# Kernel tuning notes

Hardware: AMD Instinct MI355X
Metric: run time of the kernel (lower is better)

Reference implementation:

```python
import jax, jax.numpy as jnp
import numpy as np

NUM_CLASSES = 80
ANCHORS = np.array([[10,13],[16,30],[33,23],[30,61],[62,45],[59,119],[116,90],[156,198],[373,326]], np.float32)
MASK = [[0,1,2],[3,4,5],[6,7,8]]
STRIDES = [8, 16, 32]
MAX_OUT = 100      # max_output_size_per_class == max_total_size
IOU_THR = 0.45
SCORE_THR = 0.25
NMS_TOPK = 128     # per-class candidate pre-selection for greedy NMS (>= MAX_OUT)


def setup_inputs() -> dict:
    key = jax.random.key(0)
    k1, k2, k3 = jax.random.split(key, 3)
    B = 16
    C = 3 * (NUM_CLASSES + 5)  # 255
    return {
        'p3': jax.random.normal(k1, (B, 80, 80, C), jnp.float32),
        'p4': jax.random.normal(k2, (B, 40, 40, C), jnp.float32),
        'p5': jax.random.normal(k3, (B, 20, 20, C), jnp.float32),
    }


def _decode(logits, anchors, stride):
    # logits: [B,H,W,3*(nc+5)] -> boxes [B,H*W*3,4] (x1y1x2y2), obj [B,M], cls [B,M,nc]
    B, H, W, _ = logits.shape
    A = anchors.shape[0]
    x = logits.reshape(B, H, W, A, NUM_CLASSES + 5)
    xy = jax.nn.sigmoid(x[..., :2])
    wh_logit = x[..., 2:4]
    obj = jax.nn.sigmoid(x[..., 4])
    cls = jax.nn.sigmoid(x[..., 5:])
    gx, gy = jnp.meshgrid(jnp.arange(W, dtype=x.dtype), jnp.arange(H, dtype=x.dtype))
    grid = jnp.stack([gx, gy], axis=-1)[:, :, None, :]  # [H,W,1,2]
    ctr = (xy + grid) * stride
    wh = jnp.exp(wh_logit) * anchors  # [B,H,W,A,2]
    box = jnp.concatenate([ctr - wh / 2.0, ctr + wh / 2.0], axis=-1)
    return box.reshape(B, -1, 4), obj.reshape(B, -1), cls.reshape(B, -1, NUM_CLASSES)


def _pairwise_iou(b):
    # b: [K,4] x1y1x2y2 -> [K,K]
    area = (b[:, 2] - b[:, 0]) * (b[:, 3] - b[:, 1])
    lt = jnp.maximum(b[:, None, :2], b[None, :, :2])
    rb = jnp.minimum(b[:, None, 2:], b[None, :, 2:])
    wh = jnp.clip(rb - lt, 0.0)
    inter = wh[..., 0] * wh[..., 1]
    return inter / (area[:, None] + area[None, :] - inter + 1e-9)


def _nms_single(boxes, scores):
    # boxes [N,4], scores [N] for one (image, class): greedy NMS on top-K candidates
    s = jnp.where(scores > SCORE_THR, scores, -1.0)
    top_s, idx = jax.lax.top_k(s, NMS_TOPK)   # sorted descending
    b = boxes[idx]                            # [K,4]
    iou = _pairwise_iou(b)                    # [K,K]
    rng = jnp.arange(NMS_TOPK)

    def body(keep, i):
        active = keep[i] & (top_s[i] > 0.0)
        sup = active & (iou[i] > IOU_THR) & (rng > i)
        return keep & ~sup, None

    keep, _ = jax.lax.scan(body, jnp.ones(NMS_TOPK, bool), rng)
    valid = keep & (top_s > 0.0)
    ss = jnp.where(valid, top_s, -1.0)
    sel_s, sel_i = jax.lax.top_k(ss, MAX_OUT)
    return b[sel_i], sel_s                    # [M,4], [M]


def _per_image(boxes, scores_cn):
    # boxes [N,4] shared across classes (q=1), scores_cn [C,N]
    cb, cs = jax.vmap(_nms_single, in_axes=(None, 0))(boxes, scores_cn)  # [C,M,4],[C,M]
    C = cs.shape[0]
    cls_id = jnp.broadcast_to(jnp.arange(C, dtype=boxes.dtype)[:, None], cs.shape)
    fs, fi = jax.lax.top_k(cs.reshape(-1), MAX_OUT)
    fb = cb.reshape(-1, 4)[fi]
    fc = cls_id.reshape(-1)[fi]
    valid = fs > 0.0
    n_valid = jnp.sum(valid).astype(jnp.int32)
    return (jnp.where(valid[:, None], fb, 0.0),
            jnp.where(valid, fs, 0.0),
            jnp.where(valid, fc, 0.0),
            n_valid)


def _forward(p3, p4, p5):
    boxes, objs, clss = [], [], []
    for logits, m, stride in zip((p3, p4, p5), MASK, STRIDES):
        b, o, c = _decode(logits, jnp.asarray(ANCHORS[m]), float(stride))
        boxes.append(b); objs.append(o); clss.append(c)
    boxes = jnp.concatenate(boxes, axis=1)   # [B,N,4]
    obj = jnp.concatenate(objs, axis=1)      # [B,N]
    cls = jnp.concatenate(clss, axis=1)      # [B,N,C]
    scores = obj[..., None] * cls            # [B,N,C]
    return jax.vmap(_per_image)(boxes, scores.transpose(0, 2, 1))


def reference(p3, p4, p5):
    # returns (boxes [B,100,4], scores [B,100], classes [B,100], valid [B])
    return _forward(p3, p4, p5)
```

## Files before the change

### kernel.cpp

```cpp
#include <hip/hip_runtime.h>
#include <stdint.h>

#define NUM_CLASSES 80
#define N_ANCH 25200
#define B_IMG 16
#define NMS_TOPK_ 128
#define MAX_OUT_ 100
#define SCORE_THR_ 0.25f
#define IOU_THR_ 0.45f
#define NBINS 2048
#define CAP 2048
#define CAPB 1024
#define CAPC 256
#define U16_THR 0x3E80u

__constant__ float c_anch[9][2] = {
    {10.f, 13.f}, {16.f, 30.f}, {33.f, 23.f},
    {30.f, 61.f}, {62.f, 45.f}, {59.f, 119.f},
    {116.f, 90.f}, {156.f, 198.f}, {373.f, 326.f}};

__device__ __forceinline__ float sigmoidf_(float x) {
    return 1.0f / (1.0f + expf(-x));
}

__device__ __forceinline__ unsigned int score_bin(unsigned int bits) {
    unsigned int bin = (bits - 0x3E800000u) >> 13;
    if (bin >= NBINS) bin = NBINS - 1;
    return bin;
}


__global__ void __launch_bounds__(256) decode_scores_u16_kernel(
    const float* __restrict__ p3, const float* __restrict__ p4,
    const float* __restrict__ p5, float* __restrict__ boxes,
    unsigned short* __restrict__ score_u) {
    int blk = blockIdx.x;
    int b = blk / 405;
    int tile = blk - b * 405;
    const float* p; int W, lvl, il0, base, ta;
    if (tile < 300)      { p = p3; W = 80; lvl = 0; ta = 64; il0 = tile * 64;         base = 0;     }
    else if (tile < 375) { p = p4; W = 40; lvl = 1; ta = 64; il0 = (tile - 300) * 64; base = 19200; }
    else                 { p = p5; W = 20; lvl = 2; ta = 40; il0 = (tile - 375) * 40; base = 24000; }
    float stride = (float)(8 << lvl);

    __shared__ float4 raw4[64 * 85 / 4];
    __shared__ float obj_sh[64];
    float* raw = (float*)raw4;
    int tid = threadIdx.x;

    const float4* src4 = (const float4*)(p + (size_t)b * ((size_t)W * W * 255) +
                                         (size_t)il0 * 85);
    int n4 = ta * 85 / 4;
    for (int k = tid; k < n4; k += 256) raw4[k] = src4[k];
    __syncthreads();

    if (tid < ta) {
        int il = il0 + tid;
        int y = il / (W * 3);
        int t = il - y * (W * 3);
        int x = t / 3;
        int a = t - x * 3;
        const float* q = &raw[tid * 85];
        float cx = (sigmoidf_(q[0]) + (float)x) * stride;
        float cy = (sigmoidf_(q[1]) + (float)y) * stride;
        float bw = expf(q[2]) * c_anch[lvl * 3 + a][0];
        float bh = expf(q[3]) * c_anch[lvl * 3 + a][1];
        int gi = base + il;
        float* bo = boxes + ((size_t)b * N_ANCH + gi) * 4;
        bo[0] = cx - bw * 0.5f; bo[1] = cy - bh * 0.5f;
        bo[2] = cx + bw * 0.5f; bo[3] = cy + bh * 0.5f;
        obj_sh[tid] = sigmoidf_(q[4]);
    }
    __syncthreads();

    int gi0 = base + il0;
    int gpc = ta >> 3;
    int ng = NUM_CLASSES * gpc;
    for (int o = tid; o < ng; o += 256) {
        int c, g;
        if (gpc == 8) { c = o >> 3; g = o & 7; }
        else          { c = o / 5;  g = o - c * 5; }
        int j = g * 8;
        unsigned int w[4];
#pragma unroll
        for (int k = 0; k < 4; ++k) {
            float s0 = obj_sh[j + 2 * k]     * sigmoidf_(raw[(j + 2 * k) * 85 + 5 + c]);
            float s1 = obj_sh[j + 2 * k + 1] * sigmoidf_(raw[(j + 2 * k + 1) * 85 + 5 + c]);
            w[k] = (__float_as_uint(s0) >> 16) | (__float_as_uint(s1) & 0xFFFF0000u);
        }
        uint4 v = {w[0], w[1], w[2], w[3]};
        *(uint4*)(score_u + ((size_t)(b * NUM_CLASSES + c)) * N_ANCH + gi0 + j) = v;
    }
}

__global__ void __launch_bounds__(256) select_topk_u16_kernel(
    const unsigned short* __restrict__ score_u,
    const float* __restrict__ p3, const float* __restrict__ p4,
    const float* __restrict__ p5,
    unsigned long long* __restrict__ topsel) {
    int bc = blockIdx.x;
    int b = bc / NUM_CLASSES;
    int c = bc - b * NUM_CLASSES;
    int tid = threadIdx.x;
    const uint4* sc = (const uint4*)(score_u + (size_t)bc * N_ANCH);

    __shared__ unsigned int hist[256];
    __shared__ unsigned long long sel[CAPB];
    __shared__ unsigned int s_cnt;
    __shared__ int s_cut;

    hist[tid] = 0u;
    if (tid == 0) s_cnt = 0u;
    __syncthreads();

    for (int i = tid; i < N_ANCH / 8; i += 256) {
        uint4 v = sc[i];
        unsigned int ww[4] = {v.x, v.y, v.z, v.w};
#pragma unroll
        for (int k = 0; k < 8; ++k) {
            unsigned int h = (ww[k >> 1] >> ((k & 1) * 16)) & 0xFFFFu;
            if (h >= U16_THR) {
                unsigned int bin = h - U16_THR;
                if (bin > 255u) bin = 255u;
                atomicAdd(&hist[bin], 1u);
            }
        }
    }
    __syncthreads();

    if (tid == 0) {
        unsigned int tot = 0; int cut = 0;
        for (int t = 255; t >= 0; --t) {
            tot += hist[t];
            if (tot >= NMS_TOPK_) { cut = t; break; }
        }
        s_cut = cut;
    }
    __syncthreads();
    unsigned int cutoff = (unsigned int)s_cut;

    for (int i = tid; i < N_ANCH / 8; i += 256) {
        uint4 v = sc[i];
        unsigned int ww[4] = {v.x, v.y, v.z, v.w};
#pragma unroll
        for (int k = 0; k < 8; ++k) {
            unsigned int h = (ww[k >> 1] >> ((k & 1) * 16)) & 0xFFFFu;
            if (h >= U16_THR) {
                unsigned int bin = h - U16_THR;
                if (bin > 255u) bin = 255u;
                if (bin >= cutoff) {
                    unsigned int pos = atomicAdd(&s_cnt, 1u);
                    if (pos < CAPB) sel[pos] = (unsigned long long)(i * 8 + k);
                }
            }
        }
    }
    __syncthreads();

    unsigned int M = s_cnt;
    if (M > CAPB) M = CAPB;

    for (unsigned int t = tid; t < M; t += 256) {
        unsigned int idx = (unsigned int)sel[t];
        const float* q;
        if (idx < 19200u)      q = p3 + (size_t)b * 1632000 + (size_t)idx * 85;
        else if (idx < 24000u) q = p4 + (size_t)b * 408000 + (size_t)(idx - 19200u) * 85;
        else                   q = p5 + (size_t)b * 102000 + (size_t)(idx - 24000u) * 85;
        float s = sigmoidf_(q[4]) * sigmoidf_(q[5 + c]);
        sel[t] = (s > SCORE_THR_)
                     ? (((unsigned long long)__float_as_uint(s) << 32) |
                        (unsigned long long)(~idx))
                     : 0ull;
    }
    __syncthreads();

    unsigned int P2 = 1;
    while (P2 < M) P2 <<= 1;
    if (P2 < 2) P2 = 2;
    for (unsigned int k = M + tid; k < P2; k += 256) sel[k] = 0ull;
    __syncthreads();

    for (unsigned int k = 2; k <= P2; k <<= 1) {
        for (unsigned int j = k >> 1; j > 0; j >>= 1) {
            for (unsigned int t = tid; t < (int)P2; t += 256) {
                unsigned int ixj = (unsigned int)t ^ j;
                if (ixj > (unsigned int)t) {
                    unsigned long long a0 = sel[t], b0 = sel[ixj];
                    bool desc = (((unsigned int)t & k) == 0);
                    if (desc ? (a0 < b0) : (a0 > b0)) { sel[t] = b0; sel[ixj] = a0; }
                }
            }
            __syncthreads();
        }
    }

    unsigned long long* dst = topsel + (size_t)bc * NMS_TOPK_;
    if (tid < NMS_TOPK_) dst[tid] = ((unsigned int)tid < M) ? sel[tid] : 0ull;
}

__global__ void __launch_bounds__(64) nms_kernel(
    const unsigned long long* __restrict__ topsel,
    const float* __restrict__ boxes,
    float* __restrict__ cls_score, float* __restrict__ cls_box) {
    int bc = blockIdx.x;
    int b = bc / NUM_CLASSES;
    unsigned int lane = threadIdx.x;

    __shared__ float bx[NMS_TOPK_][8];

    const unsigned long long* src = topsel + (size_t)bc * NMS_TOPK_;
    unsigned long long e0 = src[lane];
    unsigned long long e1 = src[64 + lane];

    bool k0 = (e0 != 0ull);
    bool k1 = (e1 != 0ull);

    float x00 = 0, y00 = 0, x01 = 0, y01 = 0, a0 = 0, sv0 = 0;
    float x10 = 0, y10 = 0, x11 = 0, y11 = 0, a1 = 0, sv1 = 0;
    if (k0) {
        unsigned int idx = ~((unsigned int)(e0 & 0xFFFFFFFFull));
        float4 bp = *(const float4*)(boxes + ((size_t)b * N_ANCH + idx) * 4);
        x00 = bp.x; y00 = bp.y; x01 = bp.z; y01 = bp.w;
        sv0 = __uint_as_float((unsigned int)(e0 >> 32));
        a0 = (x01 - x00) * (y01 - y00);
    }
    if (k1) {
        unsigned int idx = ~((unsigned int)(e1 & 0xFFFFFFFFull));
        float4 bp = *(const float4*)(boxes + ((size_t)b * N_ANCH + idx) * 4);
        x10 = bp.x; y10 = bp.y; x11 = bp.z; y11 = bp.w;
        sv1 = __uint_as_float((unsigned int)(e1 >> 32));
        a1 = (x11 - x10) * (y11 - y10);
    }
    {
        float4 v0 = {x00, y00, x01, y01};
        float4 v1 = {x10, y10, x11, y11};
        *(float4*)&bx[lane][0] = v0;
        *(float4*)&bx[64 + lane][0] = v1;
    }
    __syncthreads();

    unsigned long long km0 = __ballot(k0);
    unsigned long long km1 = __ballot(k1);
    for (unsigned int i = 0; i < NMS_TOPK_; ++i) {
        bool ki = ((((i < 64) ? km0 : km1) >> (i & 63)) & 1ull) != 0ull;
        if (ki) {
            float4 rb = *(const float4*)&bx[i][0];
            float ra = (rb.z - rb.x) * (rb.w - rb.y);
            if (k0 && lane > i) {
                float lx = fmaxf(rb.x, x00), ly = fmaxf(rb.y, y00);
                float rx = fminf(rb.z, x01), ry = fminf(rb.w, y01);
                float w = fmaxf(rx - lx, 0.f), h = fmaxf(ry - ly, 0.f);
                float inter = w * h;
                float iou = inter / (ra + a0 - inter + 1e-9f);
                if (iou > IOU_THR_) k0 = false;
            }
            if (k1 && (64 + lane) > i) {
                float lx = fmaxf(rb.x, x10), ly = fmaxf(rb.y, y10);
                float rx = fminf(rb.z, x11), ry = fminf(rb.w, y11);
                float w = fmaxf(rx - lx, 0.f), h = fmaxf(ry - ly, 0.f);
                float inter = w * h;
                float iou = inter / (ra + a1 - inter + 1e-9f);
                if (iou > IOU_THR_) k1 = false;
            }
            km0 = __ballot(k0);
            km1 = __ballot(k1);
        }
    }

    float* scd = cls_score + (size_t)bc * MAX_OUT_;
    float* bod = cls_box + (size_t)bc * (MAX_OUT_ * 4);
    int n0 = __popcll(km0);
    int n = n0 + __popcll(km1);
    if (k0) {
        int pos = __popcll(km0 & ((1ull << lane) - 1ull));
        if (pos < MAX_OUT_) {
            scd[pos] = sv0;
            bod[pos * 4 + 0] = x00; bod[pos * 4 + 1] = y00;
            bod[pos * 4 + 2] = x01; bod[pos * 4 + 3] = y01;
        }
    }
    if (k1) {
        int pos = n0 + __popcll(km1 & ((1ull << lane) - 1ull));
        if (pos < MAX_OUT_) {
            scd[pos] = sv1;
            bod[pos * 4 + 0] = x10; bod[pos * 4 + 1] = y10;
            bod[pos * 4 + 2] = x11; bod[pos * 4 + 3] = y11;
        }
    }
    int start = n < MAX_OUT_ ? n : MAX_OUT_;
    for (int p2 = start + (int)lane; p2 < MAX_OUT_; p2 += 64) {
        scd[p2] = -1.0f;
        bod[p2 * 4 + 0] = 0.f; bod[p2 * 4 + 1] = 0.f;
        bod[p2 * 4 + 2] = 0.f; bod[p2 * 4 + 3] = 0.f;
    }
}

__global__ void __launch_bounds__(256) final_fast_kernel(
    const float* __restrict__ cls_score, const float* __restrict__ cls_box,
    float* __restrict__ out) {
    int b = blockIdx.x;
    int tid = threadIdx.x;
    const int NC = NUM_CLASSES * MAX_OUT_;
    const float* sc = cls_score + (size_t)b * NC;

    __shared__ unsigned int hist[NBINS];
    __shared__ unsigned int segsum[256];
    __shared__ unsigned long long keys[CAPC];
    __shared__ unsigned int s_cnt, s_tot;
    __shared__ int s_cut;

    for (int k = tid; k < NBINS; k += 256) hist[k] = 0u;
    if (tid == 0) s_cnt = 0u;
    __syncthreads();

    for (int k = tid; k < NC; k += 256) {
        float s = sc[k];
        if (s > 0.0f) atomicAdd(&hist[score_bin(__float_as_uint(s))], 1u);
    }
    __syncthreads();

    unsigned int ss = 0;
    for (int k = 0; k < 8; ++k) ss += hist[tid * 8 + k];
    segsum[tid] = ss;
    __syncthreads();
    if (tid == 0) {
        unsigned int total = 0;
        for (int t = 0; t < 256; ++t) total += segsum[t];
        s_tot = total;
        unsigned int tot = 0; int cut = 0; int t = 255;
        for (; t >= 0; --t) {
            if (tot + segsum[t] >= MAX_OUT_) break;
            tot += segsum[t];
        }
        if (t >= 0) {
            int j = 7;
            for (; j >= 0; --j) { tot += hist[t * 8 + j]; if (tot >= MAX_OUT_) break; }
            if (j < 0) j = 0;
            cut = t * 8 + j;
        }
        s_cut = cut;
    }
    __syncthreads();
    unsigned int cutoff = (unsigned int)s_cut;

    for (int k = tid; k < NC; k += 256) {
        float s = sc[k];
        if (s > 0.0f && score_bin(__float_as_uint(s)) >= cutoff) {
            unsigned int pos = atomicAdd(&s_cnt, 1u);
            if (pos < CAPC) {
                keys[pos] = ((unsigned long long)__float_as_uint(s) << 32) |
                            (unsigned long long)(~(unsigned int)k);
            }
        }
    }
    __syncthreads();

    unsigned int M = s_cnt;
    if (M > CAPC) M = CAPC;
    unsigned int P2 = 1;
    while (P2 < M) P2 <<= 1;
    if (P2 < 2) P2 = 2;
    for (unsigned int k = M + tid; k < P2; k += 256) keys[k] = 0ull;
    __syncthreads();

    for (unsigned int k = 2; k <= P2; k <<= 1) {
        for (unsigned int j = k >> 1; j > 0; j >>= 1) {
            for (unsigned int t = (unsigned int)tid; t < P2; t += 256) {
                unsigned int ixj = t ^ j;
                if (ixj > t) {
                    unsigned long long a0 = keys[t], b0 = keys[ixj];
                    bool desc = ((t & k) == 0);
                    if (desc ? (a0 < b0) : (a0 > b0)) { keys[t] = b0; keys[ixj] = a0; }
                }
            }
            __syncthreads();
        }
    }

    float* ob = out;
    float* os = out + B_IMG * MAX_OUT_ * 4;
    float* oc = os + B_IMG * MAX_OUT_;
    float* on = oc + B_IMG * MAX_OUT_;

    unsigned int K = M < MAX_OUT_ ? M : MAX_OUT_;
    if (tid < MAX_OUT_) {
        if ((unsigned int)tid < K) {
            unsigned long long kk = keys[tid];
            unsigned int flat = ~((unsigned int)(kk & 0xFFFFFFFFull));
            float sv = __uint_as_float((unsigned int)(kk >> 32));
            const float* bp = cls_box + ((size_t)b * NC + flat) * 4;
            os[b * MAX_OUT_ + tid] = sv;
            oc[b * MAX_OUT_ + tid] = (float)(flat / MAX_OUT_);
            ob[(b * MAX_OUT_ + tid) * 4 + 0] = bp[0];
            ob[(b * MAX_OUT_ + tid) * 4 + 1] = bp[1];
            ob[(b * MAX_OUT_ + tid) * 4 + 2] = bp[2];
            ob[(b * MAX_OUT_ + tid) * 4 + 3] = bp[3];
        } else {
            os[b * MAX_OUT_ + tid] = 0.0f;
            oc[b * MAX_OUT_ + tid] = 0.0f;
            ob[(b * MAX_OUT_ + tid) * 4 + 0] = 0.0f;
            ob[(b * MAX_OUT_ + tid) * 4 + 1] = 0.0f;
            ob[(b * MAX_OUT_ + tid) * 4 + 2] = 0.0f;
            ob[(b * MAX_OUT_ + tid) * 4 + 3] = 0.0f;
        }
    }
    if (tid == 0) {
        unsigned int nv = s_tot < MAX_OUT_ ? s_tot : MAX_OUT_;
        on[b] = (float)nv;
    }
}


__global__ void __launch_bounds__(256) decode_kernel(
    const float* __restrict__ p3, const float* __restrict__ p4,
    const float* __restrict__ p5, float* __restrict__ boxes,
    float* __restrict__ obj) {
    int gid = blockIdx.x * blockDim.x + threadIdx.x;
    if (gid >= B_IMG * N_ANCH) return;
    int b = gid / N_ANCH;
    int i = gid - b * N_ANCH;
    const float* p; int W, il, lvl; float stride;
    if (i < 19200)      { p = p3; W = 80; il = i;         lvl = 0; stride = 8.f;  }
    else if (i < 24000) { p = p4; W = 40; il = i - 19200; lvl = 1; stride = 16.f; }
    else                { p = p5; W = 20; il = i - 24000; lvl = 2; stride = 32.f; }
    int y = il / (W * 3);
    int t = il - y * W * 3;
    int x = t / 3;
    int a = t - x * 3;
    const float* q = p + ((((size_t)b * W + y) * W + x) * 255 + a * 85);
    float cx = (sigmoidf_(q[0]) + (float)x) * stride;
    float cy = (sigmoidf_(q[1]) + (float)y) * stride;
    float bw = expf(q[2]) * c_anch[lvl * 3 + a][0];
    float bh = expf(q[3]) * c_anch[lvl * 3 + a][1];
    float* bo = boxes + (size_t)gid * 4;
    bo[0] = cx - bw * 0.5f; bo[1] = cy - bh * 0.5f;
    bo[2] = cx + bw * 0.5f; bo[3] = cy + bh * 0.5f;
    obj[gid] = sigmoidf_(q[4]);
}

__device__ __forceinline__ float cand_score(
    const float* __restrict__ p3, const float* __restrict__ p4,
    const float* __restrict__ p5, const float* __restrict__ obj,
    int b, int c, int i) {
    const float* p; int W, il;
    if (i < 19200)      { p = p3; W = 80; il = i;         }
    else if (i < 24000) { p = p4; W = 40; il = i - 19200; }
    else                { p = p5; W = 20; il = i - 24000; }
    int y = il / (W * 3);
    int t = il - y * W * 3;
    int x = t / 3;
    int a = t - x * 3;
    float cl = p[(((size_t)b * W + y) * W + x) * 255 + a * 85 + 5 + c];
    return obj[b * N_ANCH + i] * sigmoidf_(cl);
}

__global__ void __launch_bounds__(256) topk_nms_kernel(
    const float* __restrict__ p3, const float* __restrict__ p4,
    const float* __restrict__ p5, const float* __restrict__ boxes,
    const float* __restrict__ obj, float* __restrict__ cls_score,
    float* __restrict__ cls_box) {
    int b = blockIdx.x / NUM_CLASSES;
    int c = blockIdx.x % NUM_CLASSES;
    int tid = threadIdx.x;

    __shared__ unsigned int hist[NBINS];
    __shared__ unsigned long long keys[CAP];
    __shared__ unsigned int s_cnt, s_cutoff;
    __shared__ float bx[NMS_TOPK_][5];
    __shared__ float bs[NMS_TOPK_];
    __shared__ int keep[NMS_TOPK_];

    for (int k = tid; k < NBINS; k += 256) hist[k] = 0u;
    if (tid == 0) s_cnt = 0u;
    __syncthreads();

    for (int i = tid; i < N_ANCH; i += 256) {
        float s = cand_score(p3, p4, p5, obj, b, c, i);
        if (s > SCORE_THR_) atomicAdd(&hist[score_bin(__float_as_uint(s))], 1u);
    }
    __syncthreads();

    if (tid == 0) {
        unsigned int total = 0;
        int cut = 0;
        for (int k = NBINS - 1; k >= 0; --k) {
            total += hist[k];
            if (total >= NMS_TOPK_) { cut = k; break; }
        }
        s_cutoff = (unsigned int)cut;
    }
    __syncthreads();
    unsigned int cutoff = s_cutoff;

    for (int i = tid; i < N_ANCH; i += 256) {
        float s = cand_score(p3, p4, p5, obj, b, c, i);
        if (s > SCORE_THR_) {
            unsigned int bits = __float_as_uint(s);
            if (score_bin(bits) >= cutoff) {
                unsigned int pos = atomicAdd(&s_cnt, 1u);
                if (pos < CAP) {
                    keys[pos] = ((unsigned long long)bits << 32) |
                                (unsigned long long)(~(unsigned int)i);
                }
            }
        }
    }
    __syncthreads();

    unsigned int M = s_cnt;
    if (M > CAP) M = CAP;
    unsigned int P2 = 1;
    while (P2 < M) P2 <<= 1;
    if (P2 < 2) P2 = 2;
    for (unsigned int k = M + tid; k < P2; k += 256) keys[k] = 0ull;
    __syncthreads();

    for (unsigned int k = 2; k <= P2; k <<= 1) {
        for (unsigned int j = k >> 1; j > 0; j >>= 1) {
            for (unsigned int t = tid; t < P2; t += 256) {
                unsigned int ixj = t ^ j;
                if (ixj > t) {
                    unsigned long long a0 = keys[t], b0 = keys[ixj];
                    bool desc = ((t & k) == 0);
                    if (desc ? (a0 < b0) : (a0 > b0)) { keys[t] = b0; keys[ixj] = a0; }
                }
            }
            __syncthreads();
        }
    }

    unsigned int K = M < NMS_TOPK_ ? M : NMS_TOPK_;
    if (tid < (int)K) {
        unsigned long long kk = keys[tid];
        unsigned int idx = ~((unsigned int)(kk & 0xFFFFFFFFull));
        const float* bp = boxes + ((size_t)b * N_ANCH + idx) * 4;
        bx[tid][0] = bp[0]; bx[tid][1] = bp[1];
        bx[tid][2] = bp[2]; bx[tid][3] = bp[3];
        bs[tid] = __uint_as_float((unsigned int)(kk >> 32));
        keep[tid] = 1;
    }
    __syncthreads();

    for (unsigned int i = 0; i < K; ++i) {
        if (keep[i]) {
            unsigned int t = (unsigned int)tid;
            if (t > i && t < K && keep[t]) {
                float ax0 = bx[i][0], ay0 = bx[i][1], ax1 = bx[i][2], ay1 = bx[i][3];
                float cx0 = bx[t][0], cy0 = bx[t][1], cx1 = bx[t][2], cy1 = bx[t][3];
                float areaA = (ax1 - ax0) * (ay1 - ay0);
                float areaB = (cx1 - cx0) * (cy1 - cy0);
                float lx = fmaxf(ax0, cx0), ly = fmaxf(ay0, cy0);
                float rx = fminf(ax1, cx1), ry = fminf(ay1, cy1);
                float w = rx - lx; if (w < 0.f) w = 0.f;
                float h = ry - ly; if (h < 0.f) h = 0.f;
                float inter = w * h;
                float iou = inter / (areaA + areaB - inter + 1e-9f);
                if (iou > IOU_THR_) keep[t] = 0;
            }
        }
        __syncthreads();
    }

    if (tid == 0) {
        float* scd = cls_score + ((size_t)b * NUM_CLASSES + c) * MAX_OUT_;
        float* bod = cls_box + ((size_t)b * NUM_CLASSES + c) * MAX_OUT_ * 4;
        int out_n = 0;
        for (unsigned int t2 = 0; t2 < K && out_n < MAX_OUT_; ++t2) {
            if (keep[t2]) {
                scd[out_n] = bs[t2];
                bod[out_n * 4 + 0] = bx[t2][0];
                bod[out_n * 4 + 1] = bx[t2][1];
                bod[out_n * 4 + 2] = bx[t2][2];
                bod[out_n * 4 + 3] = bx[t2][3];
                out_n++;
            }
        }
        for (; out_n < MAX_OUT_; ++out_n) {
            scd[out_n] = -1.0f;
            bod[out_n * 4 + 0] = 0.f; bod[out_n * 4 + 1] = 0.f;
            bod[out_n * 4 + 2] = 0.f; bod[out_n * 4 + 3] = 0.f;
        }
    }
}

extern "C" void kernel_launch(void* const* d_in, const int* in_sizes, int n_in,
                              void* d_out, int out_size, void* d_ws, size_t ws_size,
                              hipStream_t stream) {
    const float* p3 = (const float*)d_in[0];
    const float* p4 = (const float*)d_in[1];
    const float* p5 = (const float*)d_in[2];

    const size_t boxesB  = (size_t)B_IMG * N_ANCH * 4 * sizeof(float);
    const size_t clsSB   = (size_t)B_IMG * NUM_CLASSES * MAX_OUT_ * sizeof(float);
    const size_t clsBB   = clsSB * 4;
    const size_t topselB = (size_t)B_IMG * NUM_CLASSES * NMS_TOPK_ * 8;
    const size_t scoreUB = (size_t)B_IMG * NUM_CLASSES * N_ANCH * 2;
    const size_t need_new = boxesB + clsSB + clsBB + topselB + scoreUB;

    char* base = (char*)d_ws;

    if (ws_size >= need_new) {
        float* boxes     = (float*)base;
        float* cls_score = (float*)(base + boxesB);
        float* cls_box   = (float*)(base + boxesB + clsSB);
        unsigned long long* topsel =
            (unsigned long long*)(base + boxesB + clsSB + clsBB);
        unsigned short* score_u =
            (unsigned short*)(base + boxesB + clsSB + clsBB + topselB);

        decode_scores_u16_kernel<<<B_IMG * 405, 256, 0, stream>>>(
            p3, p4, p5, boxes, score_u);
        select_topk_u16_kernel<<<B_IMG * NUM_CLASSES, 256, 0, stream>>>(
            score_u, p3, p4, p5, topsel);
        nms_kernel<<<B_IMG * NUM_CLASSES, 64, 0, stream>>>(
            topsel, boxes, cls_score, cls_box);
        final_fast_kernel<<<B_IMG, 256, 0, stream>>>(cls_score, cls_box, (float*)d_out);
    } else {
        float* boxes = (float*)base;
        float* obj = boxes + (size_t)B_IMG * N_ANCH * 4;
        float* cls_score = obj + (size_t)B_IMG * N_ANCH;
        float* cls_box = cls_score + (size_t)B_IMG * NUM_CLASSES * MAX_OUT_;

        int tot = B_IMG * N_ANCH;
        decode_kernel<<<(tot + 255) / 256, 256, 0, stream>>>(p3, p4, p5, boxes, obj);
        topk_nms_kernel<<<B_IMG * NUM_CLASSES, 256, 0, stream>>>(
            p3, p4, p5, boxes, obj, cls_score, cls_box);
        final_fast_kernel<<<B_IMG, 256, 0, stream>>>(cls_score, cls_box, (float*)d_out);
    }
}
```

Baseline: 312.1 us.

## Split decode into per-wave 16-anchor chunks and privatize histogram per wave

Decode now gives each 64-lane wave its own 16-anchor chunk. It loads, decodes boxes with four lanes per anchor, and writes packed u16 scores with no block-wide barriers, relying only on wave-local fences. This aims to remove __syncthreads stalls and the idle-thread phases of the old 256-thread, 64-anchor tiles. The top-k selection kernel also gets one shared histogram per wave, merged afterwards, to cut atomic contention. The per-wave sync assumes wave64 lockstep execution through LDS, which is fragile but holds on CDNA.

```diff
diff --git a/kernel.cpp b/kernel.cpp
--- a/kernel.cpp
+++ b/kernel.cpp
@@ -13,6 +13,7 @@
 #define CAPB 1024
 #define CAPC 256
 #define U16_THR 0x3E80u
+#define CHUNKS_PER_IMG 1575
 
 __constant__ float c_anch[9][2] = {
     {10.f, 13.f}, {16.f, 30.f}, {33.f, 23.f},
@@ -30,66 +31,80 @@
 }
 
 
-__global__ void __launch_bounds__(256) decode_scores_u16_kernel(
+__global__ void __launch_bounds__(256) decode_wave_kernel(
     const float* __restrict__ p3, const float* __restrict__ p4,
     const float* __restrict__ p5, float* __restrict__ boxes,
     unsigned short* __restrict__ score_u) {
-    int blk = blockIdx.x;
-    int b = blk / 405;
-    int tile = blk - b * 405;
-    const float* p; int W, lvl, il0, base, ta;
-    if (tile < 300)      { p = p3; W = 80; lvl = 0; ta = 64; il0 = tile * 64;         base = 0;     }
-    else if (tile < 375) { p = p4; W = 40; lvl = 1; ta = 64; il0 = (tile - 300) * 64; base = 19200; }
-    else                 { p = p5; W = 20; lvl = 2; ta = 40; il0 = (tile - 375) * 40; base = 24000; }
+    int wave = threadIdx.x >> 6;
+    int lane = threadIdx.x & 63;
+    int chunk = blockIdx.x * 4 + wave;
+    int b = chunk / CHUNKS_PER_IMG;
+    int ci = chunk - b * CHUNKS_PER_IMG;
+    const float* p; int W, lvl, il0, base;
+    if (ci < 1200)      { p = p3; W = 80; lvl = 0; il0 = ci * 16;          base = 0;     }
+    else if (ci < 1500) { p = p4; W = 40; lvl = 1; il0 = (ci - 1200) * 16; base = 19200; }
+    else                { p = p5; W = 20; lvl = 2; il0 = (ci - 1500) * 16; base = 24000; }
     float stride = (float)(8 << lvl);
 
-    __shared__ float4 raw4[64 * 85 / 4];
-    __shared__ float obj_sh[64];
-    float* raw = (float*)raw4;
-    int tid = threadIdx.x;
-
-    const float4* src4 = (const float4*)(p + (size_t)b * ((size_t)W * W * 255) +
-                                         (size_t)il0 * 85);
-    int n4 = ta * 85 / 4;
-    for (int k = tid; k < n4; k += 256) raw4[k] = src4[k];
-    __syncthreads();
-
-    if (tid < ta) {
-        int il = il0 + tid;
+    __shared__ float raw_s[4][16 * 85];
+    __shared__ float obj_s[4][16];
+    float* raw = raw_s[wave];
+    float* obj_sh = obj_s[wave];
+
+    {
+        const float4* src4 = (const float4*)(p + (size_t)b * ((size_t)W * W * 255) +
+                                             (size_t)il0 * 85);
+        float4* raw4 = (float4*)raw;
+#pragma unroll
+        for (int k = 0; k < 6; ++k) {
+            int idx = lane + k * 64;
+            if (idx < 340) raw4[idx] = src4[idx];
+        }
+    }
+    __threadfence_block();
+
+    {
+        int a = lane >> 2;
+        int comp = lane & 3;
+        int il = il0 + a;
         int y = il / (W * 3);
         int t = il - y * (W * 3);
         int x = t / 3;
-        int a = t - x * 3;
-        const float* q = &raw[tid * 85];
+        int an = t - x * 3;
+        const float* q = &raw[a * 85];
         float cx = (sigmoidf_(q[0]) + (float)x) * stride;
         float cy = (sigmoidf_(q[1]) + (float)y) * stride;
-        float bw = expf(q[2]) * c_anch[lvl * 3 + a][0];
-        float bh = expf(q[3]) * c_anch[lvl * 3 + a][1];
-        int gi = base + il;
-        float* bo = boxes + ((size_t)b * N_ANCH + gi) * 4;
-        bo[0] = cx - bw * 0.5f; bo[1] = cy - bh * 0.5f;
-        bo[2] = cx + bw * 0.5f; bo[3] = cy + bh * 0.5f;
-        obj_sh[tid] = sigmoidf_(q[4]);
-    }
-    __syncthreads();
+        float bw = expf(q[2]) * c_anch[lvl * 3 + an][0];
+        float bh = expf(q[3]) * c_anch[lvl * 3 + an][1];
+        float v;
+        if (comp == 0)      v = cx - bw * 0.5f;
+        else if (comp == 1) v = cy - bh * 0.5f;
+        else if (comp == 2) v = cx + bw * 0.5f;
+        else                v = cy + bh * 0.5f;
+        boxes[((size_t)b * N_ANCH + base + il) * 4 + comp] = v;
+        if (comp == 0) obj_sh[a] = sigmoidf_(q[4]);
+    }
+    __threadfence_block();
 
     int gi0 = base + il0;
-    int gpc = ta >> 3;
-    int ng = NUM_CLASSES * gpc;
-    for (int o = tid; o < ng; o += 256) {
-        int c, g;
-        if (gpc == 8) { c = o >> 3; g = o & 7; }
-        else          { c = o / 5;  g = o - c * 5; }
-        int j = g * 8;
-        unsigned int w[4];
+    int h = lane & 1;
+    int c0 = lane >> 1;
+    int j0 = h * 8;
 #pragma unroll
-        for (int k = 0; k < 4; ++k) {
-            float s0 = obj_sh[j + 2 * k]     * sigmoidf_(raw[(j + 2 * k) * 85 + 5 + c]);
-            float s1 = obj_sh[j + 2 * k + 1] * sigmoidf_(raw[(j + 2 * k + 1) * 85 + 5 + c]);
-            w[k] = (__float_as_uint(s0) >> 16) | (__float_as_uint(s1) & 0xFFFF0000u);
-        }
-        uint4 v = {w[0], w[1], w[2], w[3]};
-        *(uint4*)(score_u + ((size_t)(b * NUM_CLASSES + c)) * N_ANCH + gi0 + j) = v;
+    for (int it = 0; it < 3; ++it) {
+        int c = it * 32 + c0;
+        if (c < NUM_CLASSES) {
+            unsigned int w[4];
+#pragma unroll
+            for (int k = 0; k < 4; ++k) {
+                int j = j0 + 2 * k;
+                float s0 = obj_sh[j]     * sigmoidf_(raw[j * 85 + 5 + c]);
+                float s1 = obj_sh[j + 1] * sigmoidf_(raw[(j + 1) * 85 + 5 + c]);
+                w[k] = (__float_as_uint(s0) >> 16) | (__float_as_uint(s1) & 0xFFFF0000u);
+            }
+            uint4 v = {w[0], w[1], w[2], w[3]};
+            *(uint4*)(score_u + ((size_t)(b * NUM_CLASSES + c)) * N_ANCH + gi0 + j0) = v;
+        }
     }
 }
 
@@ -102,36 +117,45 @@
     int b = bc / NUM_CLASSES;
     int c = bc - b * NUM_CLASSES;
     int tid = threadIdx.x;
+    int wave = tid >> 6;
     const uint4* sc = (const uint4*)(score_u + (size_t)bc * N_ANCH);
 
-    __shared__ unsigned int hist[256];
+    __shared__ unsigned int hist[4][256];
     __shared__ unsigned long long sel[CAPB];
     __shared__ unsigned int s_cnt;
     __shared__ int s_cut;
 
-    hist[tid] = 0u;
+#pragma unroll
+    for (int wv = 0; wv < 4; ++wv) hist[wv][tid & 255] = 0u;
     if (tid == 0) s_cnt = 0u;
     __syncthreads();
 
+    unsigned int* myhist = hist[wave];
     for (int i = tid; i < N_ANCH / 8; i += 256) {
         uint4 v = sc[i];
         unsigned int ww[4] = {v.x, v.y, v.z, v.w};
 #pragma unroll
         for (int k = 0; k < 8; ++k) {
-            unsigned int h = (ww[k >> 1] >> ((k & 1) * 16)) & 0xFFFFu;
-            if (h >= U16_THR) {
-                unsigned int bin = h - U16_THR;
+            unsigned int hh = (ww[k >> 1] >> ((k & 1) * 16)) & 0xFFFFu;
+            if (hh >= U16_THR) {
+                unsigned int bin = hh - U16_THR;
                 if (bin > 255u) bin = 255u;
-                atomicAdd(&hist[bin], 1u);
-            }
-        }
+                atomicAdd(&myhist[bin], 1u);
+            }
+        }
+    }
+    __syncthreads();
+
+    {
+        unsigned int m = hist[0][tid] + hist[1][tid] + hist[2][tid] + hist[3][tid];
+        hist[0][tid] = m;
     }
     __syncthreads();
 
     if (tid == 0) {
         unsigned int tot = 0; int cut = 0;
         for (int t = 255; t >= 0; --t) {
-            tot += hist[t];
+            tot += hist[0][t];
             if (tot >= NMS_TOPK_) { cut = t; break; }
         }
         s_cut = cut;
@@ -144,9 +168,9 @@
         unsigned int ww[4] = {v.x, v.y, v.z, v.w};
 #pragma unroll
         for (int k = 0; k < 8; ++k) {
-            unsigned int h = (ww[k >> 1] >> ((k & 1) * 16)) & 0xFFFFu;
-            if (h >= U16_THR) {
-                unsigned int bin = h - U16_THR;
+            unsigned int hh = (ww[k >> 1] >> ((k & 1) * 16)) & 0xFFFFu;
+            if (hh >= U16_THR) {
+                unsigned int bin = hh - U16_THR;
                 if (bin > 255u) bin = 255u;
                 if (bin >= cutoff) {
                     unsigned int pos = atomicAdd(&s_cnt, 1u);
@@ -608,7 +632,7 @@
         unsigned short* score_u =
             (unsigned short*)(base + boxesB + clsSB + clsBB + topselB);
 
-        decode_scores_u16_kernel<<<B_IMG * 405, 256, 0, stream>>>(
+        decode_wave_kernel<<<(B_IMG * CHUNKS_PER_IMG) / 4, 256, 0, stream>>>(
             p3, p4, p5, boxes, score_u);
         select_topk_u16_kernel<<<B_IMG * NUM_CLASSES, 256, 0, stream>>>(
             score_u, p3, p4, p5, topsel);
```

Result: no change. 310.2 us (-0.6%).
